# Kernel tuning notes

Hardware: AMD Instinct MI355X
Metric: run time of the kernel (lower is better)

The kernel has to match this reference:

```python
import jax, jax.numpy as jnp
import numpy as np

# static config (matches init_kwargs)
NH, NKV, E, K = 16, 4, 8, 2
CAP_FACTOR = 1.25
LN_EPS = 1e-5


def _layer_norm(x, w, b):
    mu = jnp.mean(x, axis=-1, keepdims=True)
    var = jnp.mean(jnp.square(x - mu), axis=-1, keepdims=True)
    return (x - mu) * jax.lax.rsqrt(var + LN_EPS) * w + b


def setup_inputs() -> dict:
    key = jax.random.key(0)
    ks = jax.random.split(key, 6)
    S, B, H, F = 2048, 1, 1024, 2048
    HD = H // NH
    qkv_out = NKV * ((NH // NKV) + 2) * HD  # 1536
    f32 = jnp.float32
    return {
        "hidden_states": jax.random.normal(ks[0], (S, B, H), f32),
        "ln1_weight": jnp.ones((H,), f32),
        "ln1_bias": jnp.zeros((H,), f32),
        "ln2_weight": jnp.ones((H,), f32),
        "ln2_bias": jnp.zeros((H,), f32),
        "qkv_weight": jax.random.normal(ks[1], (qkv_out, H), f32) * 0.02,
        "proj_weight": jax.random.normal(ks[2], (H, H), f32) * 0.02,
        "router_weight": jax.random.normal(ks[3], (H, E), f32) * 0.02,
        "moe_w1": jax.random.normal(ks[4], (E, H, F), f32) * 0.02,
        "moe_w2": jax.random.normal(ks[5], (F and E, F, H), f32)[:E] * 0.02 if False else jax.random.normal(ks[5], (E, F, H), f32) * 0.02,
    }


def reference(hidden_states, ln1_weight, ln1_bias, ln2_weight, ln2_bias,
              qkv_weight, proj_weight, router_weight, moe_w1, moe_w2):
    S, B, H = hidden_states.shape
    HD = H // NH
    q_per_kv = NH // NKV
    # ---- attention block (cp_size=1: all-to-alls are identity) ----
    ln1 = _layer_norm(hidden_states, ln1_weight, ln1_bias)
    qkv = jnp.einsum('sbh,oh->sbo', ln1, qkv_weight)
    qkv = qkv.reshape(S, B, NKV, (q_per_kv + 2) * HD)
    q = qkv[..., : q_per_kv * HD].reshape(S, B, NH, HD)
    k = qkv[..., q_per_kv * HD:(q_per_kv + 1) * HD]          # [S,B,NKV,HD]
    v = qkv[..., (q_per_kv + 1) * HD:]                        # [S,B,NKV,HD]
    qb = jnp.transpose(q, (1, 2, 0, 3)).reshape(B, NKV, q_per_kv, S, HD)
    kb = jnp.transpose(k, (1, 2, 0, 3))                       # [B,NKV,S,HD]
    vb = jnp.transpose(v, (1, 2, 0, 3))
    scale = 1.0 / np.sqrt(HD).astype(np.float32)
    scores = jnp.einsum('bgqsd,bgtd->bgqst', qb, kb) * scale  # [B,NKV,qpk,S,S]
    causal = jnp.tril(jnp.ones((S, S), bool))
    scores = jnp.where(causal, scores, jnp.finfo(scores.dtype).min)
    attn = jax.nn.softmax(scores, axis=-1)
    ao = jnp.einsum('bgqst,bgtd->bgqsd', attn, vb)
    ao = ao.reshape(B, NH, S, HD)
    ao = jnp.transpose(ao, (2, 0, 1, 3)).reshape(S, B, H)
    proj = jnp.einsum('sbh,oh->sbo', ao, proj_weight)
    h1 = hidden_states + proj
    # ---- MoE block (ep_size=1: uniform all-to-all is identity) ----
    ln2 = _layer_norm(h1, ln2_weight, ln2_bias)
    x = ln2.reshape(-1, H)                                    # [N,H]
    N = x.shape[0]
    logits = x @ router_weight                                # linear(x, router_weight.t())
    probs = jax.nn.softmax(logits, axis=-1)
    top_p, top_i = jax.lax.top_k(probs, K)
    top_p = top_p / jnp.sum(top_p, axis=-1, keepdims=True)
    exp_idx = top_i.reshape(-1)                               # [N*K]
    exp_p = top_p.reshape(-1)
    # stable sort by expert id, capacity-padded dispatch
    order = jnp.argsort(exp_idx, stable=True)
    sorted_exp = exp_idx[order]
    counts = jnp.bincount(exp_idx, length=E)
    offsets = jnp.concatenate([jnp.zeros((1,), counts.dtype), jnp.cumsum(counts)[:-1]])
    within = jnp.arange(N * K) - offsets[sorted_exp]
    cap = int(np.ceil(N * K / E * CAP_FACTOR))
    T = E * cap
    valid = within < cap
    dst = jnp.where(valid, sorted_exp * cap + within, T)      # T = out-of-bounds -> dropped
    padded_tokens = jnp.zeros((T, H), x.dtype).at[dst].set(x[order // K], mode='drop')
    padded_probs = jnp.zeros((T,), exp_p.dtype).at[dst].set(exp_p[order], mode='drop')
    padded_tid = jnp.zeros((T,), jnp.int32).at[dst].set((order // K).astype(jnp.int32), mode='drop')
    # grouped expert GEMMs: [E,cap,H] x [E,H,F] -> gelu -> [E,cap,H]
    xt = padded_tokens.reshape(E, cap, H)
    fc1 = jax.nn.gelu(jnp.einsum('ech,ehf->ecf', xt, moe_w1))
    fc2 = jnp.einsum('ecf,efh->ech', fc1, moe_w2).reshape(T, H)
    weighted = fc2 * padded_probs[:, None]                    # pad slots have prob 0
    moe_out = jnp.zeros((N, H), hidden_states.dtype).at[padded_tid].add(weighted)
    return h1 + moe_out.reshape(S, B, H)
```

## Files before the change

### kernel.cpp

```cpp
#include <hip/hip_runtime.h>
#include <hip/hip_bf16.h>
#include <stdint.h>

#define S_LEN 2048
#define HDIM  1024
#define NHEAD 16
#define NKVH  4
#define HEADD 64
#define QKV_O 1536
#define NEXP  8
#define TOPK  2
#define CAP   640
#define TCAP  (NEXP*CAP)
#define FDIM  2048
#define LOG2E 1.44269504088896f
#define NCHUNK 40
#define ATTN_BLOCKS (NCHUNK*NHEAD)
#define FUSED_TRANSP 3072

typedef __bf16 bf16x8 __attribute__((ext_vector_type(8)));
typedef float  f32x4  __attribute__((ext_vector_type(4)));
typedef unsigned int u32;
typedef u32 u32x4 __attribute__((ext_vector_type(4)));
typedef u32 u32x2 __attribute__((ext_vector_type(2)));
typedef unsigned short u16;
typedef u16 u16x8 __attribute__((ext_vector_type(8)));

__device__ __forceinline__ void gload16(const __bf16* g, __bf16* l) {
    __builtin_amdgcn_global_load_lds(
        (const __attribute__((address_space(1))) u32*)g,
        (__attribute__((address_space(3))) u32*)l, 16, 0, 0);
}

__device__ __constant__ const signed char c_strip[NCHUNK] =
    {0,1,2,3, 4,4, 5,5, 6,6, 7,7, 8,8,8, 9,9,9, 10,10,10, 11,11,11,
     12,12,12,12, 13,13,13,13, 14,14,14,14, 15,15,15,15};
__device__ __constant__ const signed char c_chunk[NCHUNK] =
    {0,0,0,0, 0,1, 0,1, 0,1, 0,1, 0,1,2, 0,1,2, 0,1,2, 0,1,2,
     0,1,2,3, 0,1,2,3, 0,1,2,3, 0,1,2,3};
__device__ __constant__ const signed char c_cbase[16] = {0,1,2,3,4,6,8,10,12,15,18,21,24,28,32,36};
__device__ __constant__ const signed char c_nch[16]   = {1,1,1,1,2,2,2,2,3,3,3,3,4,4,4,4};

__global__ __launch_bounds__(256)
void prep_kernel(const float* __restrict__ hidden, const float* __restrict__ ln1w,
                 const float* __restrict__ ln1bb, const float* __restrict__ qkvW,
                 const float* __restrict__ projW, __bf16* __restrict__ ln1o,
                 __bf16* __restrict__ projWb, __bf16* __restrict__ qkvWb) {
    const int b = blockIdx.x, tid = threadIdx.x;
    if (b < S_LEN) {
        __shared__ float red[256];
        const float* x = hidden + (size_t)b * HDIM;
        float xr[4];
        #pragma unroll
        for (int j = 0; j < 4; ++j) xr[j] = x[tid + 256*j];
        float s = xr[0] + xr[1] + xr[2] + xr[3];
        red[tid] = s; __syncthreads();
        for (int st = 128; st > 0; st >>= 1) { if (tid < st) red[tid] += red[tid+st]; __syncthreads(); }
        float mu = red[0] / HDIM; __syncthreads();
        float v = 0.f;
        #pragma unroll
        for (int j = 0; j < 4; ++j) { float d = xr[j]-mu; v += d*d; }
        red[tid] = v; __syncthreads();
        for (int st = 128; st > 0; st >>= 1) { if (tid < st) red[tid] += red[tid+st]; __syncthreads(); }
        float rstd = rsqrtf(red[0]/HDIM + 1e-5f);
        #pragma unroll
        for (int j = 0; j < 4; ++j) {
            int i = tid + 256*j;
            ln1o[(size_t)b*HDIM + i] = (__bf16)((xr[j]-mu)*rstd*ln1w[i] + ln1bb[i]);
        }
        return;
    }
    const float* src; __bf16* dst; int i;
    if (b < S_LEN + 768) { src = qkvW; dst = qkvWb; i = (b - S_LEN)*256 + tid; }
    else                 { src = projW; dst = projWb; i = (b - S_LEN - 768)*256 + tid; }
    const float4* s = (const float4*)src + (size_t)i*2;
    float4 a = s[0], b4 = s[1];
    __bf16 tmp[8] = {(__bf16)a.x,(__bf16)a.y,(__bf16)a.z,(__bf16)a.w,
                     (__bf16)b4.x,(__bf16)b4.y,(__bf16)b4.z,(__bf16)b4.w};
    *(u32x4*)(dst + (size_t)i*8) = *(u32x4*)tmp;
}

template<int EPI>
__global__ __launch_bounds__(256)
void gemm_bf16_kernel(const __bf16* __restrict__ A, const __bf16* __restrict__ Bt,
                      const float* __restrict__ R, void* __restrict__ Cout,
                      int N, int K, long sA, long sB, long sC) {
    __shared__ __bf16 As[128*64];
    __shared__ __bf16 Bs[128*64];
    const int e = blockIdx.z;
    A  += (size_t)e * sA;
    Bt += (size_t)e * sB;
    const int m0 = blockIdx.y*128, n0 = blockIdx.x*128;
    const int tid = threadIdx.x;
    const int lane = tid & 63, w = tid >> 6;
    const int lr = lane & 15, lg = lane >> 4;
    const int wr = w >> 1, wc = w & 1;
    const int srow8 = lane >> 3, sg = lane & 7;
    f32x4 acc[4][4] = {};
    for (int k0 = 0; k0 < K; k0 += 64) {
        __syncthreads();
        #pragma unroll
        for (int i = 0; i < 4; ++i) {
            int row = 32*w + 8*i + srow8;
            int src_g = sg ^ (row & 7);
            gload16(A  + (size_t)(m0+row)*K + k0 + src_g*8,
                    (__bf16*)((char*)As + (32*w + 8*i)*128));
            gload16(Bt + (size_t)(n0+row)*K + k0 + src_g*8,
                    (__bf16*)((char*)Bs + (32*w + 8*i)*128));
        }
        __syncthreads();
        #pragma unroll
        for (int ks = 0; ks < 2; ++ks) {
            bf16x8 af[4], bfr[4];
            #pragma unroll
            for (int mi = 0; mi < 4; ++mi) {
                int row = wr*64 + mi*16 + lr;
                af[mi] = *(const bf16x8*)((const char*)As + ((row*128 + (lg+4*ks)*16) ^ ((row&7)<<4)));
            }
            #pragma unroll
            for (int ni = 0; ni < 4; ++ni) {
                int row = wc*64 + ni*16 + lr;
                bfr[ni] = *(const bf16x8*)((const char*)Bs + ((row*128 + (lg+4*ks)*16) ^ ((row&7)<<4)));
            }
            #pragma unroll
            for (int mi = 0; mi < 4; ++mi)
                #pragma unroll
                for (int ni = 0; ni < 4; ++ni)
                    acc[mi][ni] = __builtin_amdgcn_mfma_f32_16x16x32_bf16(af[mi], bfr[ni], acc[mi][ni], 0,0,0);
        }
    }
    #pragma unroll
    for (int mi = 0; mi < 4; ++mi) {
        #pragma unroll
        for (int ni = 0; ni < 4; ++ni) {
            #pragma unroll
            for (int r = 0; r < 4; ++r) {
                int row = m0 + wr*64 + mi*16 + lg*4 + r;
                int col = n0 + wc*64 + ni*16 + lr;
                float v = acc[mi][ni][r];
                if (EPI == 1) v += R[(size_t)row*N + col];
                if (EPI == 2) {
                    float t = 0.7978845608028654f * (v + 0.044715f*v*v*v);
                    v = 0.5f * v * (1.f + tanhf(t));
                }
                if (EPI == 2 || EPI == 3)
                    ((__bf16*)Cout)[(size_t)e*sC + (size_t)row*N + col] = (__bf16)v;
                else
                    ((float*)Cout)[(size_t)e*sC + (size_t)row*N + col] = v;
            }
        }
    }
}

template<int EPI>
__global__ __launch_bounds__(256)
void gemm64_bf16_kernel(const __bf16* __restrict__ A, const __bf16* __restrict__ Bt,
                        const float* __restrict__ R, void* __restrict__ Cout,
                        int N, int K, long sA, long sB, long sC) {
    __shared__ __bf16 As[64*64];
    __shared__ __bf16 Bs[128*64];
    const int e = blockIdx.z;
    A  += (size_t)e * sA;
    Bt += (size_t)e * sB;
    const int m0 = blockIdx.y*64, n0 = blockIdx.x*128;
    const int tid = threadIdx.x;
    const int lane = tid & 63, w = tid >> 6;
    const int lr = lane & 15, lg = lane >> 4;
    const int srow8 = lane >> 3, sg = lane & 7;
    f32x4 acc[4][2] = {};
    for (int k0 = 0; k0 < K; k0 += 64) {
        __syncthreads();
        #pragma unroll
        for (int i = 0; i < 2; ++i) {
            int row = 16*w + 8*i + srow8;
            int src_g = sg ^ (row & 7);
            gload16(A + (size_t)(m0+row)*K + k0 + src_g*8,
                    (__bf16*)((char*)As + (16*w + 8*i)*128));
        }
        #pragma unroll
        for (int i = 0; i < 4; ++i) {
            int row = 32*w + 8*i + srow8;
            int src_g = sg ^ (row & 7);
            gload16(Bt + (size_t)(n0+row)*K + k0 + src_g*8,
                    (__bf16*)((char*)Bs + (32*w + 8*i)*128));
        }
        __syncthreads();
        #pragma unroll
        for (int ks = 0; ks < 2; ++ks) {
            bf16x8 af[4], bfr[2];
            #pragma unroll
            for (int mi = 0; mi < 4; ++mi) {
                int row = mi*16 + lr;
                af[mi] = *(const bf16x8*)((const char*)As + ((row*128 + (lg+4*ks)*16) ^ ((row&7)<<4)));
            }
            #pragma unroll
            for (int ni = 0; ni < 2; ++ni) {
                int row = w*32 + ni*16 + lr;
                bfr[ni] = *(const bf16x8*)((const char*)Bs + ((row*128 + (lg+4*ks)*16) ^ ((row&7)<<4)));
            }
            #pragma unroll
            for (int mi = 0; mi < 4; ++mi)
                #pragma unroll
                for (int ni = 0; ni < 2; ++ni)
                    acc[mi][ni] = __builtin_amdgcn_mfma_f32_16x16x32_bf16(af[mi], bfr[ni], acc[mi][ni], 0,0,0);
        }
    }
    #pragma unroll
    for (int mi = 0; mi < 4; ++mi) {
        #pragma unroll
        for (int ni = 0; ni < 2; ++ni) {
            #pragma unroll
            for (int r = 0; r < 4; ++r) {
                int row = m0 + mi*16 + lg*4 + r;
                int col = n0 + w*32 + ni*16 + lr;
                float v = acc[mi][ni][r];
                if (EPI == 1) v += R[(size_t)row*N + col];
                if (EPI == 2) {
                    float t = 0.7978845608028654f * (v + 0.044715f*v*v*v);
                    v = 0.5f * v * (1.f + tanhf(t));
                }
                if (EPI == 2 || EPI == 3)
                    ((__bf16*)Cout)[(size_t)e*sC + (size_t)row*N + col] = (__bf16)v;
                else
                    ((float*)Cout)[(size_t)e*sC + (size_t)row*N + col] = v;
            }
        }
    }
}

__global__ __launch_bounds__(256)
void proj_transp_kernel(const __bf16* __restrict__ A, const __bf16* __restrict__ Bt,
                        const float* __restrict__ R, float* __restrict__ Cout,
                        const float* __restrict__ w2, __bf16* __restrict__ w2t) {
    __shared__ __attribute__((aligned(16))) char smem[24576];
    const int bid = blockIdx.x, tid = threadIdx.x;
    if (bid >= 256) {
        float (*t)[65] = (float(*)[65])smem;
        const int tile = 6144 + (bid - 256);
        const int tt = tile - 4096;
        const int e = tt >> 9, rem = tt & 511;
        const int K = FDIM, N = HDIM;
        const int n0 = (rem & 15) * 64, k0 = (rem >> 4) * 64;
        const float* src = w2 + (size_t)e*K*N;
        __bf16* dst = w2t + (size_t)e*K*N;
        const int r = tid >> 4, c4 = (tid & 15) * 4;
        #pragma unroll
        for (int i = 0; i < 4; ++i) {
            float4 v = *(const float4*)(src + (size_t)(k0 + r + 16*i)*N + n0 + c4);
            t[r+16*i][c4+0] = v.x; t[r+16*i][c4+1] = v.y;
            t[r+16*i][c4+2] = v.z; t[r+16*i][c4+3] = v.w;
        }
        __syncthreads();
        const int rn = tid >> 3, kc = (tid & 7) * 8;
        #pragma unroll
        for (int i = 0; i < 2; ++i) {
            int n = rn + 32*i;
            __bf16 tmp[8];
            #pragma unroll
            for (int j = 0; j < 8; ++j) tmp[j] = (__bf16)t[kc+j][n];
            *(u32x4*)(dst + (size_t)(n0+n)*K + k0 + kc) = *(u32x4*)tmp;
        }
        return;
    }
    __bf16* As = (__bf16*)smem;
    __bf16* Bs = (__bf16*)(smem + 8192);
    const int N = HDIM, K = HDIM;
    const int m0 = (bid >> 3)*64, n0 = (bid & 7)*128;
    const int lane = tid & 63, w = tid >> 6;
    const int lr = lane & 15, lg = lane >> 4;
    const int srow8 = lane >> 3, sg = lane & 7;
    f32x4 acc[4][2] = {};
    for (int k0 = 0; k0 < K; k0 += 64) {
        __syncthreads();
        #pragma unroll
        for (int i = 0; i < 2; ++i) {
            int row = 16*w + 8*i + srow8;
            int src_g = sg ^ (row & 7);
            gload16(A + (size_t)(m0+row)*K + k0 + src_g*8,
                    (__bf16*)((char*)As + (16*w + 8*i)*128));
        }
        #pragma unroll
        for (int i = 0; i < 4; ++i) {
            int row = 32*w + 8*i + srow8;
            int src_g = sg ^ (row & 7);
            gload16(Bt + (size_t)(n0+row)*K + k0 + src_g*8,
                    (__bf16*)((char*)Bs + (32*w + 8*i)*128));
        }
        __syncthreads();
        #pragma unroll
        for (int ks = 0; ks < 2; ++ks) {
            bf16x8 af[4], bfr[2];
            #pragma unroll
            for (int mi = 0; mi < 4; ++mi) {
                int row = mi*16 + lr;
                af[mi] = *(const bf16x8*)((const char*)As + ((row*128 + (lg+4*ks)*16) ^ ((row&7)<<4)));
            }
            #pragma unroll
            for (int ni = 0; ni < 2; ++ni) {
                int row = w*32 + ni*16 + lr;
                bfr[ni] = *(const bf16x8*)((const char*)Bs + ((row*128 + (lg+4*ks)*16) ^ ((row&7)<<4)));
            }
            #pragma unroll
            for (int mi = 0; mi < 4; ++mi)
                #pragma unroll
                for (int ni = 0; ni < 2; ++ni)
                    acc[mi][ni] = __builtin_amdgcn_mfma_f32_16x16x32_bf16(af[mi], bfr[ni], acc[mi][ni], 0,0,0);
        }
    }
    #pragma unroll
    for (int mi = 0; mi < 4; ++mi) {
        #pragma unroll
        for (int ni = 0; ni < 2; ++ni) {
            #pragma unroll
            for (int r = 0; r < 4; ++r) {
                int row = m0 + mi*16 + lg*4 + r;
                int col = n0 + w*32 + ni*16 + lr;
                Cout[(size_t)row*N + col] = acc[mi][ni][r] + R[(size_t)row*N + col];
            }
        }
    }
}

__global__ __launch_bounds__(512)
void attn_transp_kernel(const __bf16* __restrict__ qkv, float* __restrict__ partO,
                        float* __restrict__ partML,
                        const float* __restrict__ w1, const float* __restrict__ w2,
                        __bf16* __restrict__ w1t, __bf16* __restrict__ w2t) {
    __shared__ __attribute__((aligned(16))) char smem[49152];
    const int bid = blockIdx.x;
    const bool is_attn = ((bid % 5) == 3) && (bid / 5 < ATTN_BLOCKS);

    if (!is_attn) {
        const int tb = bid - min(ATTN_BLOCKS, (bid + 2) / 5);
        const int half = threadIdx.x >> 8, t256 = threadIdx.x & 255;
        float (*t)[65] = (float(*)[65])(smem + half*16640);
        const int tile = tb*2 + half;
        const float* src; __bf16* dst; int K, N, n0, k0;
        if (tile < 4096) {
            int e = tile >> 9, rem = tile & 511;
            K = HDIM; N = FDIM; n0 = (rem & 31) * 64; k0 = (rem >> 5) * 64;
            src = w1 + (size_t)e*K*N; dst = w1t + (size_t)e*K*N;
        } else {
            int tt = tile - 4096; int e = tt >> 9, rem = tt & 511;
            K = FDIM; N = HDIM; n0 = (rem & 15) * 64; k0 = (rem >> 4) * 64;
            src = w2 + (size_t)e*K*N; dst = w2t + (size_t)e*K*N;
        }
        const int r = t256 >> 4, c4 = (t256 & 15) * 4;
        #pragma unroll
        for (int i = 0; i < 4; ++i) {
            float4 v = *(const float4*)(src + (size_t)(k0 + r + 16*i)*N + n0 + c4);
            t[r+16*i][c4+0] = v.x; t[r+16*i][c4+1] = v.y;
            t[r+16*i][c4+2] = v.z; t[r+16*i][c4+3] = v.w;
        }
        __syncthreads();
        const int rn = t256 >> 3, kc = (t256 & 7) * 8;
        #pragma unroll
        for (int i = 0; i < 2; ++i) {
            int n = rn + 32*i;
            __bf16 tmp[8];
            #pragma unroll
            for (int j = 0; j < 8; ++j) tmp[j] = (__bf16)t[kc+j][n];
            *(u32x4*)(dst + (size_t)(n0+n)*K + k0 + kc) = *(u32x4*)tmp;
        }
        return;
    }

    __bf16* Kls = (__bf16*)smem;
    __bf16* Vls = (__bf16*)(smem + 16384);
    const int a = bid / 5;
    const int cx = a % NCHUNK;
    const int h  = a / NCHUNK;
    const int hg = h >> 2, qi = h & 3;
    const int qb = c_strip[cx];
    const int t0 = 4 * c_chunk[cx];
    const int t1 = min(qb + 1, t0 + 4);
    const int q0 = qb * 128;
    const int tid  = threadIdx.x;
    const int w    = tid >> 6;
    const int lane = tid & 63;
    const int lr   = lane & 15;
    const int lg   = lane >> 4;

    const int krow = tid >> 2, kc = (tid & 3) * 2;
    const int va = tid & 63,  dg  = tid >> 6;
    u32x4 kreg[2]; u16x8 vreg[2];

    const __bf16* kbase = qkv + hg*384 + 256;
    const __bf16* vbase = qkv + hg*384 + 320;

#define ISSUE(T) do { \
        const __bf16* kp = kbase + (size_t)((T)*128 + krow)*QKV_O + kc*8; \
        kreg[0] = *(const u32x4*)(kp); \
        kreg[1] = *(const u32x4*)(kp + 8); \
        const __bf16* vp = vbase + (size_t)((T)*128 + 2*va)*QKV_O + dg*8; \
        vreg[0] = *(const u16x8*)(vp); \
        vreg[1] = *(const u16x8*)(vp + QKV_O); \
    } while(0)

#define COMMIT() do { \
        char* Kb = (char*)Kls; \
        *(u32x4*)(Kb + ((krow*128 + (kc+0)*16) ^ ((krow&7)<<4))) = kreg[0]; \
        *(u32x4*)(Kb + ((krow*128 + (kc+1)*16) ^ ((krow&7)<<4))) = kreg[1]; \
        char* Vb = (char*)Vls; \
        _Pragma("unroll") \
        for (int j = 0; j < 8; ++j) { \
            int d = dg*8 + j; \
            u32 u = ((u32)vreg[1][j] << 16) | vreg[0][j]; \
            *(u32*)(Vb + ((d*256 + va*4) ^ ((d&7)<<4))) = u; \
        } \
    } while(0)

    const int qrow = q0 + w*16 + lr;
    const __bf16* qp = qkv + (size_t)qrow*QKV_O + hg*384 + qi*64;
    bf16x8 qfrag[2];
    #pragma unroll
    for (int ks = 0; ks < 2; ++ks) {
        bf16x8 qr = *(const bf16x8*)(qp + ks*32 + lg*8);
        #pragma unroll
        for (int j = 0; j < 8; ++j) qfrag[ks][j] = (__bf16)((float)qr[j] * 0.125f);
    }
    bf16x8 ones;
    #pragma unroll
    for (int j = 0; j < 8; ++j) ones[j] = (__bf16)1.0f;

    f32x4 oacc[4] = {};
    f32x4 lcol = {};
    float mrow[4] = {-INFINITY,-INFINITY,-INFINITY,-INFINITY};

    ISSUE(t0);
    for (int t = t0; t < t1; ++t) {
        __syncthreads();
        COMMIT();
        if (t+1 < t1) ISSUE(t+1);
        __syncthreads();

        f32x4 sacc[8] = {};
        const char* Kb = (const char*)Kls;
        #pragma unroll
        for (int f = 0; f < 8; ++f) {
            int row = lr + 16*f;
            int swz = (row & 7) << 4;
            #pragma unroll
            for (int ks = 0; ks < 2; ++ks) {
                bf16x8 kf = *(const bf16x8*)(Kb + ((row*128 + (lg*8+32*ks)*2) ^ swz));
                sacc[f] = __builtin_amdgcn_mfma_f32_16x16x32_bf16(qfrag[ks], kf, sacc[f], 0,0,0);
            }
        }
        if (t == qb) {
            #pragma unroll
            for (int f = 0; f < 8; ++f)
                #pragma unroll
                for (int r = 0; r < 4; ++r)
                    if (lr + 16*f > 16*w + 4*lg + r) sacc[f][r] = -INFINITY;
        }
        float tm[4];
        #pragma unroll
        for (int r = 0; r < 4; ++r) {
            float a2 = fmaxf(fmaxf(sacc[0][r], sacc[1][r]), fmaxf(sacc[2][r], sacc[3][r]));
            float b2 = fmaxf(fmaxf(sacc[4][r], sacc[5][r]), fmaxf(sacc[6][r], sacc[7][r]));
            tm[r] = fmaxf(a2, b2);
        }
        #pragma unroll
        for (int msk = 1; msk < 16; msk <<= 1)
            #pragma unroll
            for (int r = 0; r < 4; ++r) tm[r] = fmaxf(tm[r], __shfl_xor(tm[r], msk, 64));
        float corr[4];
        #pragma unroll
        for (int r = 0; r < 4; ++r) {
            float mn = fmaxf(mrow[r], tm[r]);
            corr[r] = exp2f((mrow[r]-mn)*LOG2E);
            mrow[r] = mn;
        }
        #pragma unroll
        for (int f = 0; f < 8; ++f)
            #pragma unroll
            for (int r = 0; r < 4; ++r)
                sacc[f][r] = exp2f((sacc[f][r]-mrow[r])*LOG2E);
        #pragma unroll
        for (int ct = 0; ct < 4; ++ct)
            #pragma unroll
            for (int r = 0; r < 4; ++r) oacc[ct][r] *= corr[r];
        #pragma unroll
        for (int r = 0; r < 4; ++r) lcol[r] *= corr[r];

        char* Pw = smem + 32768 + w*2048;
        const char* Vb = (const char*)Vls;
        #pragma unroll
        for (int half = 0; half < 2; ++half) {
            #pragma unroll
            for (int f = 0; f < 4; ++f)
                #pragma unroll
                for (int r = 0; r < 4; ++r) {
                    int row = 4*lg + r, col = lr + 16*f;
                    *(__bf16*)(Pw + ((row*128 + col*2) ^ ((row&7)<<4))) = (__bf16)sacc[4*half+f][r];
                }
            bf16x8 pa[2];
            #pragma unroll
            for (int ks = 0; ks < 2; ++ks)
                pa[ks] = *(const bf16x8*)(Pw + ((lr*128 + (lg*8+32*ks)*2) ^ ((lr&7)<<4)));
            #pragma unroll
            for (int ks = 0; ks < 2; ++ks)
                lcol = __builtin_amdgcn_mfma_f32_16x16x32_bf16(pa[ks], ones, lcol, 0,0,0);
            #pragma unroll
            for (int ct = 0; ct < 4; ++ct) {
                int row = lr + 16*ct;
                int swz = (row & 7) << 4;
                #pragma unroll
                for (int ks = 0; ks < 2; ++ks) {
                    int gks = 2*half + ks;
                    bf16x8 vf = *(const bf16x8*)(Vb + ((row*256 + (lg*8+32*gks)*2) ^ swz));
                    oacc[ct] = __builtin_amdgcn_mfma_f32_16x16x32_bf16(pa[ks], vf, oacc[ct], 0,0,0);
                }
            }
        }
    }
    const int p = h*NCHUNK + cx;
    float* po = partO + (size_t)p * (128*64);
    #pragma unroll
    for (int ct = 0; ct < 4; ++ct)
        #pragma unroll
        for (int r = 0; r < 4; ++r)
            po[(16*w + 4*lg + r)*64 + 16*ct + lr] = oacc[ct][r];
    if (lr == 0) {
        float* pm = partML + (size_t)p * 256;
        #pragma unroll
        for (int r = 0; r < 4; ++r) {
            pm[(16*w + 4*lg + r)*2    ] = mrow[r];
            pm[(16*w + 4*lg + r)*2 + 1] = lcol[r];
        }
    }
#undef ISSUE
#undef COMMIT
}

__global__ __launch_bounds__(256)
void attn_combine_kernel(const float* __restrict__ partO, const float* __restrict__ partML,
                         __bf16* __restrict__ ao) {
    const int rb = blockIdx.x, h = blockIdx.y;
    const int row0 = rb*8;
    const int qb = row0 >> 7;
    const int nc = c_nch[qb], cb = c_cbase[qb];
    const int tid = threadIdx.x;
    const int rl = tid >> 5, d2 = (tid & 31) * 2;
    const int grow = row0 + rl;
    const int srow = grow & 127;
    const int pbase = h*NCHUNK + cb;
    float mv[4], lv[4];
    float M = -INFINITY;
    for (int c = 0; c < nc; ++c) {
        const float* pm = partML + (size_t)(pbase+c)*256 + srow*2;
        mv[c] = pm[0]; lv[c] = pm[1];
        M = fmaxf(M, mv[c]);
    }
    float L = 0.f, a0 = 0.f, a1 = 0.f;
    for (int c = 0; c < nc; ++c) {
        float wc = exp2f((mv[c]-M)*LOG2E);
        L += wc * lv[c];
        const float* po = partO + (size_t)(pbase+c)*(128*64) + srow*64 + d2;
        a0 += wc * po[0];
        a1 += wc * po[1];
    }
    float inv = 1.f / L;
    __bf16 o2[2] = {(__bf16)(a0*inv), (__bf16)(a1*inv)};
    *(u32*)(ao + (size_t)grow*HDIM + h*64 + d2) = *(u32*)o2;
}

__global__ __launch_bounds__(256)
void ln2_router_kernel(const float* __restrict__ h1, const float* __restrict__ w,
                       const float* __restrict__ b, const float* __restrict__ rw,
                       __bf16* __restrict__ x2b, int* __restrict__ expi,
                       float* __restrict__ expp) {
    const int t = blockIdx.x, tid = threadIdx.x;
    __shared__ float red[256];
    __shared__ float red8[256][8];
    const float* x = h1 + (size_t)t*HDIM;
    float xr[4];
    #pragma unroll
    for (int j = 0; j < 4; ++j) xr[j] = x[tid + 256*j];
    float s = xr[0] + xr[1] + xr[2] + xr[3];
    red[tid] = s; __syncthreads();
    for (int st = 128; st > 0; st >>= 1) { if (tid < st) red[tid] += red[tid+st]; __syncthreads(); }
    float mu = red[0] / HDIM; __syncthreads();
    float v = 0.f;
    #pragma unroll
    for (int j = 0; j < 4; ++j) { float d = xr[j]-mu; v += d*d; }
    red[tid] = v; __syncthreads();
    for (int st = 128; st > 0; st >>= 1) { if (tid < st) red[tid] += red[tid+st]; __syncthreads(); }
    float rstd = rsqrtf(red[0]/HDIM + 1e-5f);
    float part[8] = {};
    #pragma unroll
    for (int j = 0; j < 4; ++j) {
        int i = tid + 256*j;
        float o = (xr[j]-mu)*rstd*w[i] + b[i];
        x2b[(size_t)t*HDIM + i] = (__bf16)o;
        const float* wp = rw + (size_t)i*NEXP;
        #pragma unroll
        for (int e2 = 0; e2 < 8; ++e2) part[e2] += o * wp[e2];
    }
    #pragma unroll
    for (int e2 = 0; e2 < 8; ++e2) red8[tid][e2] = part[e2];
    __syncthreads();
    for (int st = 128; st > 0; st >>= 1) {
        if (tid < st)
            #pragma unroll
            for (int e2 = 0; e2 < 8; ++e2) red8[tid][e2] += red8[tid+st][e2];
        __syncthreads();
    }
    if (tid == 0) {
        float lg[8];
        #pragma unroll
        for (int e2 = 0; e2 < 8; ++e2) lg[e2] = red8[0][e2];
        int i0 = 0;
        for (int e2 = 1; e2 < 8; ++e2) if (lg[e2] > lg[i0]) i0 = e2;
        int i1 = -1;
        for (int e2 = 0; e2 < 8; ++e2) { if (e2 == i0) continue; if (i1 < 0 || lg[e2] > lg[i1]) i1 = e2; }
        float p1 = __expf(lg[i1] - lg[i0]);
        float inv = 1.f / (1.f + p1);
        expi[t*2]   = i0; expi[t*2+1] = i1;
        expp[t*2]   = inv; expp[t*2+1] = p1 * inv;
    }
}

__global__ __launch_bounds__(256)
void dst_fast_kernel(const int* __restrict__ expi, int* __restrict__ dst) {
    __shared__ int hist[256][9];
    const int tid = threadIdx.x;
    int ev[16];
    #pragma unroll
    for (int i = 0; i < 16; i += 4)
        *(int4*)(ev+i) = *(const int4*)(expi + tid*16 + i);
    int cnt[8] = {};
    #pragma unroll
    for (int i = 0; i < 16; ++i)
        #pragma unroll
        for (int e = 0; e < 8; ++e) cnt[e] += (ev[i] == e);
    #pragma unroll
    for (int e = 0; e < 8; ++e) hist[tid][e] = cnt[e];
    __syncthreads();
    const int w = tid >> 6, lane = tid & 63;
    #pragma unroll
    for (int rep = 0; rep < 2; ++rep) {
        int e = w + rep*4;
        int h0 = hist[4*lane+0][e], h1 = hist[4*lane+1][e],
            h2 = hist[4*lane+2][e], h3 = hist[4*lane+3][e];
        int s = h0+h1+h2+h3, inc = s;
        #pragma unroll
        for (int off = 1; off < 64; off <<= 1) {
            int v = __shfl_up(inc, off, 64);
            if (lane >= off) inc += v;
        }
        int excl = inc - s;
        hist[4*lane+0][e] = excl;
        hist[4*lane+1][e] = excl + h0;
        hist[4*lane+2][e] = excl + h0 + h1;
        hist[4*lane+3][e] = excl + h0 + h1 + h2;
    }
    __syncthreads();
    int run[8];
    #pragma unroll
    for (int e = 0; e < 8; ++e) run[e] = hist[tid][e];
    int out[16];
    #pragma unroll
    for (int i = 0; i < 16; ++i) {
        int e = ev[i], within = 0;
        #pragma unroll
        for (int e2 = 0; e2 < 8; ++e2)
            if (e == e2) { within = run[e2]; run[e2]++; }
        out[i] = (within < CAP) ? (e*CAP + within) : -1;
    }
    #pragma unroll
    for (int i = 0; i < 16; i += 4)
        *(int4*)(dst + tid*16 + i) = *(const int4*)(out+i);
}

__global__ void scatter_kernel(const __bf16* __restrict__ x2b, const int* __restrict__ dst,
                               __bf16* __restrict__ xt) {
    int s = blockIdx.x;
    int d = dst[s];
    if (d < 0) return;
    int t = s >> 1;
    int i = threadIdx.x;
    u32x2 v = *(const u32x2*)(x2b + (size_t)t*HDIM + i*4);
    *(u32x2*)(xt + (size_t)d*HDIM + i*4) = v;
}

__global__ void combine_kernel(const float* __restrict__ h1, const float* __restrict__ fc2,
                               const int* __restrict__ dst, const float* __restrict__ expp,
                               float* __restrict__ out) {
    int t = blockIdx.x;
    int d0 = dst[t*2], d1 = dst[t*2+1];
    float p0 = expp[t*2], p1 = expp[t*2+1];
    int i = threadIdx.x * 4;
    float4 v = *(const float4*)(h1 + (size_t)t*HDIM + i);
    if (d0 >= 0) {
        float4 f = *(const float4*)(fc2 + (size_t)d0*HDIM + i);
        v.x += p0*f.x; v.y += p0*f.y; v.z += p0*f.z; v.w += p0*f.w;
    }
    if (d1 >= 0) {
        float4 f = *(const float4*)(fc2 + (size_t)d1*HDIM + i);
        v.x += p1*f.x; v.y += p1*f.y; v.z += p1*f.z; v.w += p1*f.w;
    }
    *(float4*)(out + (size_t)t*HDIM + i) = v;
}

extern "C" void kernel_launch(void* const* d_in, const int* in_sizes, int n_in,
                              void* d_out, int out_size, void* d_ws, size_t ws_size,
                              hipStream_t stream) {
    const float* hidden = (const float*)d_in[0];
    const float* ln1w   = (const float*)d_in[1];
    const float* ln1b_  = (const float*)d_in[2];
    const float* ln2w   = (const float*)d_in[3];
    const float* ln2b_  = (const float*)d_in[4];
    const float* qkvW   = (const float*)d_in[5];
    const float* projW  = (const float*)d_in[6];
    const float* routW  = (const float*)d_in[7];
    const float* w1     = (const float*)d_in[8];
    const float* w2     = (const float*)d_in[9];
    float* out = (float*)d_out;

    char* base = (char*)d_ws;
    __bf16* w1t    = (__bf16*)(base);
    __bf16* w2t    = (__bf16*)(base + 33554432);
    __bf16* ln1b   = (__bf16*)(base);
    __bf16* qkvWb  = (__bf16*)(base + 4194304);
    char* B0 = base + 67108864;
    float*  h1   = (float*)(B0);
    __bf16* xtb  = (__bf16*)(B0 + 8388608);
    __bf16* fc1b = (__bf16*)(B0 + 18874368);
    float*  fc2  = (float*)(B0 + 39845888);
    __bf16* x2b    = (__bf16*)fc2;
    __bf16* qkvb   = (__bf16*)((char*)fc2 + 4194304);
    __bf16* aob    = (__bf16*)((char*)fc2 + 10485760);
    __bf16* projWb = (__bf16*)((char*)fc2 + 14680064);
    int*    expi = (int*)(B0 + 60817408);
    int*    dsts = (int*)(B0 + 60833792);
    float*  expp = (float*)(B0 + 60850176);
    float*  partML = (float*)xtb;
    float*  partO  = (float*)fc1b;

    prep_kernel<<<S_LEN + 768 + 512, 256, 0, stream>>>(
        hidden, ln1w, ln1b_, qkvW, projW, ln1b, projWb, qkvWb);
    gemm64_bf16_kernel<3><<<dim3(QKV_O/128, S_LEN/64, 1), 256, 0, stream>>>(
        ln1b, qkvWb, nullptr, qkvb, QKV_O, HDIM, 0, 0, 0);
    attn_transp_kernel<<<ATTN_BLOCKS + FUSED_TRANSP, 512, 0, stream>>>(
        qkvb, partO, partML, w1, w2, w1t, w2t);
    attn_combine_kernel<<<dim3(S_LEN/8, NHEAD), 256, 0, stream>>>(partO, partML, aob);
    proj_transp_kernel<<<256 + 2048, 256, 0, stream>>>(
        aob, projWb, hidden, h1, w2, w2t);
    ln2_router_kernel<<<S_LEN, 256, 0, stream>>>(h1, ln2w, ln2b_, routW, x2b, expi, expp);
    dst_fast_kernel<<<1, 256, 0, stream>>>(expi, dsts);
    scatter_kernel<<<S_LEN*TOPK, 256, 0, stream>>>(x2b, dsts, xtb);
    gemm_bf16_kernel<2><<<dim3(FDIM/128, CAP/128, NEXP), 256, 0, stream>>>(
        xtb, w1t, nullptr, fc1b, FDIM, HDIM,
        (long)CAP*HDIM, (long)FDIM*HDIM, (long)CAP*FDIM);
    gemm64_bf16_kernel<0><<<dim3(HDIM/128, CAP/64, NEXP), 256, 0, stream>>>(
        fc1b, w2t, nullptr, fc2, HDIM, FDIM,
        (long)CAP*FDIM, (long)FDIM*HDIM, (long)CAP*HDIM);
    combine_kernel<<<S_LEN, 256, 0, stream>>>(h1, fc2, dsts, expp, out);
}
```

Baseline: 222.0 us.

## Fuse QKV GEMM with weight transposes and store expert fc2 output as bf16

The standalone QKV GEMM is replaced by a combined kernel that interleaves its 384 GEMM tiles with 1024 w2 transpose tiles, so the weight conversion work is spread across three kernels (qkv, attention, proj) and overlaps with compute. The second expert GEMM now writes bf16 instead of fp32, and combine reads bf16, halving that intermediate's memory traffic. Workspace buffers are relaid out to fit the smaller fc2. The bf16 fc2 adds rounding error, and the transpose tile ranges must be partitioned exactly across the kernels.

Measured after the change: 221.4 us, median of 4. No clear change (-0.3%).

```diff
diff --git a/kernel.cpp b/kernel.cpp
--- a/kernel.cpp
+++ b/kernel.cpp
@@ -16,7 +16,7 @@
 #define LOG2E 1.44269504088896f
 #define NCHUNK 40
 #define ATTN_BLOCKS (NCHUNK*NHEAD)
-#define FUSED_TRANSP 3072
+#define ATTN_TRANSP 2560
 
 typedef __bf16 bf16x8 __attribute__((ext_vector_type(8)));
 typedef float  f32x4  __attribute__((ext_vector_type(4)));
@@ -40,6 +40,41 @@
      0,1,2,3, 0,1,2,3, 0,1,2,3, 0,1,2,3};
 __device__ __constant__ const signed char c_cbase[16] = {0,1,2,3,4,6,8,10,12,15,18,21,24,28,32,36};
 __device__ __constant__ const signed char c_nch[16]   = {1,1,1,1,2,2,2,2,3,3,3,3,4,4,4,4};
+
+__device__ __forceinline__ void transp_tile(const float* __restrict__ w1,
+                                            const float* __restrict__ w2,
+                                            __bf16* __restrict__ w1t,
+                                            __bf16* __restrict__ w2t,
+                                            int tile, int tid, char* smem) {
+    float (*t)[65] = (float(*)[65])smem;
+    const float* src; __bf16* dst; int K, N, n0, k0;
+    if (tile < 4096) {
+        int e = tile >> 9, rem = tile & 511;
+        K = HDIM; N = FDIM; n0 = (rem & 31) * 64; k0 = (rem >> 5) * 64;
+        src = w1 + (size_t)e*K*N; dst = w1t + (size_t)e*K*N;
+    } else {
+        int tt = tile - 4096; int e = tt >> 9, rem = tt & 511;
+        K = FDIM; N = HDIM; n0 = (rem & 15) * 64; k0 = (rem >> 4) * 64;
+        src = w2 + (size_t)e*K*N; dst = w2t + (size_t)e*K*N;
+    }
+    const int r = tid >> 4, c4 = (tid & 15) * 4;
+    #pragma unroll
+    for (int i = 0; i < 4; ++i) {
+        float4 v = *(const float4*)(src + (size_t)(k0 + r + 16*i)*N + n0 + c4);
+        t[r+16*i][c4+0] = v.x; t[r+16*i][c4+1] = v.y;
+        t[r+16*i][c4+2] = v.z; t[r+16*i][c4+3] = v.w;
+    }
+    __syncthreads();
+    const int rn = tid >> 3, kc = (tid & 7) * 8;
+    #pragma unroll
+    for (int i = 0; i < 2; ++i) {
+        int n = rn + 32*i;
+        __bf16 tmp[8];
+        #pragma unroll
+        for (int j = 0; j < 8; ++j) tmp[j] = (__bf16)t[kc+j][n];
+        *(u32x4*)(dst + (size_t)(n0+n)*K + k0 + kc) = *(u32x4*)tmp;
+    }
+}
 
 __global__ __launch_bounds__(256)
 void prep_kernel(const float* __restrict__ hidden, const float* __restrict__ ln1w,
@@ -229,37 +264,85 @@
 }
 
 __global__ __launch_bounds__(256)
+void qkv_transp_kernel(const __bf16* __restrict__ A, const __bf16* __restrict__ Bt,
+                       __bf16* __restrict__ Cout,
+                       const float* __restrict__ w1, const float* __restrict__ w2,
+                       __bf16* __restrict__ w1t, __bf16* __restrict__ w2t) {
+    __shared__ __attribute__((aligned(16))) char smem[24576];
+    const int bid = blockIdx.x, tid = threadIdx.x;
+    const bool is_gemm = ((bid % 3) == 1) && (bid / 3 < 384);
+    if (!is_gemm) {
+        const int tb = bid - min(384, (bid + 2) / 3);
+        transp_tile(w1, w2, w1t, w2t, 4096 + tb, tid, smem);
+        return;
+    }
+    __bf16* As = (__bf16*)smem;
+    __bf16* Bs = (__bf16*)(smem + 8192);
+    const int g = bid / 3;
+    const int N = QKV_O, K = HDIM;
+    const int m0 = (g / 12)*64, n0 = (g % 12)*128;
+    const int lane = tid & 63, w = tid >> 6;
+    const int lr = lane & 15, lg = lane >> 4;
+    const int srow8 = lane >> 3, sg = lane & 7;
+    f32x4 acc[4][2] = {};
+    for (int k0 = 0; k0 < K; k0 += 64) {
+        __syncthreads();
+        #pragma unroll
+        for (int i = 0; i < 2; ++i) {
+            int row = 16*w + 8*i + srow8;
+            int src_g = sg ^ (row & 7);
+            gload16(A + (size_t)(m0+row)*K + k0 + src_g*8,
+                    (__bf16*)((char*)As + (16*w + 8*i)*128));
+        }
+        #pragma unroll
+        for (int i = 0; i < 4; ++i) {
+            int row = 32*w + 8*i + srow8;
+            int src_g = sg ^ (row & 7);
+            gload16(Bt + (size_t)(n0+row)*K + k0 + src_g*8,
+                    (__bf16*)((char*)Bs + (32*w + 8*i)*128));
+        }
+        __syncthreads();
+        #pragma unroll
+        for (int ks = 0; ks < 2; ++ks) {
+            bf16x8 af[4], bfr[2];
+            #pragma unroll
+            for (int mi = 0; mi < 4; ++mi) {
+                int row = mi*16 + lr;
+                af[mi] = *(const bf16x8*)((const char*)As + ((row*128 + (lg+4*ks)*16) ^ ((row&7)<<4)));
+            }
+            #pragma unroll
+            for (int ni = 0; ni < 2; ++ni) {
+                int row = w*32 + ni*16 + lr;
+                bfr[ni] = *(const bf16x8*)((const char*)Bs + ((row*128 + (lg+4*ks)*16) ^ ((row&7)<<4)));
+            }
+            #pragma unroll
+            for (int mi = 0; mi < 4; ++mi)
+                #pragma unroll
+                for (int ni = 0; ni < 2; ++ni)
+                    acc[mi][ni] = __builtin_amdgcn_mfma_f32_16x16x32_bf16(af[mi], bfr[ni], acc[mi][ni], 0,0,0);
+        }
+    }
+    #pragma unroll
+    for (int mi = 0; mi < 4; ++mi)
+        #pragma unroll
+        for (int ni = 0; ni < 2; ++ni)
+            #pragma unroll
+            for (int r = 0; r < 4; ++r) {
+                int row = m0 + mi*16 + lg*4 + r;
+                int col = n0 + w*32 + ni*16 + lr;
+                Cout[(size_t)row*N + col] = (__bf16)acc[mi][ni][r];
+            }
+}
+
+__global__ __launch_bounds__(256)
 void proj_transp_kernel(const __bf16* __restrict__ A, const __bf16* __restrict__ Bt,
                         const float* __restrict__ R, float* __restrict__ Cout,
-                        const float* __restrict__ w2, __bf16* __restrict__ w2t) {
+                        const float* __restrict__ w1, const float* __restrict__ w2,
+                        __bf16* __restrict__ w1t, __bf16* __restrict__ w2t) {
     __shared__ __attribute__((aligned(16))) char smem[24576];
     const int bid = blockIdx.x, tid = threadIdx.x;
     if (bid >= 256) {
-        float (*t)[65] = (float(*)[65])smem;
-        const int tile = 6144 + (bid - 256);
-        const int tt = tile - 4096;
-        const int e = tt >> 9, rem = tt & 511;
-        const int K = FDIM, N = HDIM;
-        const int n0 = (rem & 15) * 64, k0 = (rem >> 4) * 64;
-        const float* src = w2 + (size_t)e*K*N;
-        __bf16* dst = w2t + (size_t)e*K*N;
-        const int r = tid >> 4, c4 = (tid & 15) * 4;
-        #pragma unroll
-        for (int i = 0; i < 4; ++i) {
-            float4 v = *(const float4*)(src + (size_t)(k0 + r + 16*i)*N + n0 + c4);
-            t[r+16*i][c4+0] = v.x; t[r+16*i][c4+1] = v.y;
-            t[r+16*i][c4+2] = v.z; t[r+16*i][c4+3] = v.w;
-        }
-        __syncthreads();
-        const int rn = tid >> 3, kc = (tid & 7) * 8;
-        #pragma unroll
-        for (int i = 0; i < 2; ++i) {
-            int n = rn + 32*i;
-            __bf16 tmp[8];
-            #pragma unroll
-            for (int j = 0; j < 8; ++j) tmp[j] = (__bf16)t[kc+j][n];
-            *(u32x4*)(dst + (size_t)(n0+n)*K + k0 + kc) = *(u32x4*)tmp;
-        }
+        transp_tile(w1, w2, w1t, w2t, 6144 + (bid - 256), tid, smem);
         return;
     }
     __bf16* As = (__bf16*)smem;
@@ -308,17 +391,15 @@
         }
     }
     #pragma unroll
-    for (int mi = 0; mi < 4; ++mi) {
-        #pragma unroll
-        for (int ni = 0; ni < 2; ++ni) {
+    for (int mi = 0; mi < 4; ++mi)
+        #pragma unroll
+        for (int ni = 0; ni < 2; ++ni)
             #pragma unroll
             for (int r = 0; r < 4; ++r) {
                 int row = m0 + mi*16 + lg*4 + r;
                 int col = n0 + w*32 + ni*16 + lr;
                 Cout[(size_t)row*N + col] = acc[mi][ni][r] + R[(size_t)row*N + col];
             }
-        }
-    }
 }
 
 __global__ __launch_bounds__(512)
@@ -333,35 +414,9 @@
     if (!is_attn) {
         const int tb = bid - min(ATTN_BLOCKS, (bid + 2) / 5);
         const int half = threadIdx.x >> 8, t256 = threadIdx.x & 255;
-        float (*t)[65] = (float(*)[65])(smem + half*16640);
-        const int tile = tb*2 + half;
-        const float* src; __bf16* dst; int K, N, n0, k0;
-        if (tile < 4096) {
-            int e = tile >> 9, rem = tile & 511;
-            K = HDIM; N = FDIM; n0 = (rem & 31) * 64; k0 = (rem >> 5) * 64;
-            src = w1 + (size_t)e*K*N; dst = w1t + (size_t)e*K*N;
-        } else {
-            int tt = tile - 4096; int e = tt >> 9, rem = tt & 511;
-            K = FDIM; N = HDIM; n0 = (rem & 15) * 64; k0 = (rem >> 4) * 64;
-            src = w2 + (size_t)e*K*N; dst = w2t + (size_t)e*K*N;
-        }
-        const int r = t256 >> 4, c4 = (t256 & 15) * 4;
-        #pragma unroll
-        for (int i = 0; i < 4; ++i) {
-            float4 v = *(const float4*)(src + (size_t)(k0 + r + 16*i)*N + n0 + c4);
-            t[r+16*i][c4+0] = v.x; t[r+16*i][c4+1] = v.y;
-            t[r+16*i][c4+2] = v.z; t[r+16*i][c4+3] = v.w;
-        }
-        __syncthreads();
-        const int rn = t256 >> 3, kc = (t256 & 7) * 8;
-        #pragma unroll
-        for (int i = 0; i < 2; ++i) {
-            int n = rn + 32*i;
-            __bf16 tmp[8];
-            #pragma unroll
-            for (int j = 0; j < 8; ++j) tmp[j] = (__bf16)t[kc+j][n];
-            *(u32x4*)(dst + (size_t)(n0+n)*K + k0 + kc) = *(u32x4*)tmp;
-        }
+        int tile0 = tb*2 + half;
+        int tile = (tile0 < 4096) ? tile0 : tile0 + 1024;
+        transp_tile(w1, w2, w1t, w2t, tile, t256, smem + half*16640);
         return;
     }
 
@@ -684,7 +739,7 @@
     *(u32x2*)(xt + (size_t)d*HDIM + i*4) = v;
 }
 
-__global__ void combine_kernel(const float* __restrict__ h1, const float* __restrict__ fc2,
+__global__ void combine_kernel(const float* __restrict__ h1, const __bf16* __restrict__ fc2b,
                                const int* __restrict__ dst, const float* __restrict__ expp,
                                float* __restrict__ out) {
     int t = blockIdx.x;
@@ -693,12 +748,16 @@
     int i = threadIdx.x * 4;
     float4 v = *(const float4*)(h1 + (size_t)t*HDIM + i);
     if (d0 >= 0) {
-        float4 f = *(const float4*)(fc2 + (size_t)d0*HDIM + i);
-        v.x += p0*f.x; v.y += p0*f.y; v.z += p0*f.z; v.w += p0*f.w;
+        u16x8 f; *(u32x2*)&f = *(const u32x2*)(fc2b + (size_t)d0*HDIM + i);
+        const __bf16* fb = (const __bf16*)&f;
+        v.x += p0*(float)fb[0]; v.y += p0*(float)fb[1];
+        v.z += p0*(float)fb[2]; v.w += p0*(float)fb[3];
     }
     if (d1 >= 0) {
-        float4 f = *(const float4*)(fc2 + (size_t)d1*HDIM + i);
-        v.x += p1*f.x; v.y += p1*f.y; v.z += p1*f.z; v.w += p1*f.w;
+        u16x8 f; *(u32x2*)&f = *(const u32x2*)(fc2b + (size_t)d1*HDIM + i);
+        const __bf16* fb = (const __bf16*)&f;
+        v.x += p1*(float)fb[0]; v.y += p1*(float)fb[1];
+        v.z += p1*(float)fb[2]; v.w += p1*(float)fb[3];
     }
     *(float4*)(out + (size_t)t*HDIM + i) = v;
 }
@@ -727,11 +786,11 @@
     float*  h1   = (float*)(B0);
     __bf16* xtb  = (__bf16*)(B0 + 8388608);
     __bf16* fc1b = (__bf16*)(B0 + 18874368);
-    float*  fc2  = (float*)(B0 + 39845888);
-    __bf16* x2b    = (__bf16*)fc2;
-    __bf16* qkvb   = (__bf16*)((char*)fc2 + 4194304);
-    __bf16* aob    = (__bf16*)((char*)fc2 + 10485760);
-    __bf16* projWb = (__bf16*)((char*)fc2 + 14680064);
+    __bf16* fc2b = (__bf16*)(B0 + 39845888);
+    __bf16* x2b    = (__bf16*)((char*)fc2b + 10485760);
+    __bf16* qkvb   = (__bf16*)((char*)fc2b + 14680064);
+    __bf16* aob    = (__bf16*)(B0 + 60817408 + 65536);
+    __bf16* projWb = (__bf16*)((char*)aob + 4194304);
     int*    expi = (int*)(B0 + 60817408);
     int*    dsts = (int*)(B0 + 60833792);
     float*  expp = (float*)(B0 + 60850176);
@@ -740,21 +799,21 @@
 
     prep_kernel<<<S_LEN + 768 + 512, 256, 0, stream>>>(
         hidden, ln1w, ln1b_, qkvW, projW, ln1b, projWb, qkvWb);
-    gemm64_bf16_kernel<3><<<dim3(QKV_O/128, S_LEN/64, 1), 256, 0, stream>>>(
-        ln1b, qkvWb, nullptr, qkvb, QKV_O, HDIM, 0, 0, 0);
-    attn_transp_kernel<<<ATTN_BLOCKS + FUSED_TRANSP, 512, 0, stream>>>(
+    qkv_transp_kernel<<<384 + 1024, 256, 0, stream>>>(
+        ln1b, qkvWb, qkvb, w1, w2, w1t, w2t);
+    attn_transp_kernel<<<ATTN_BLOCKS + ATTN_TRANSP, 512, 0, stream>>>(
         qkvb, partO, partML, w1, w2, w1t, w2t);
     attn_combine_kernel<<<dim3(S_LEN/8, NHEAD), 256, 0, stream>>>(partO, partML, aob);
     proj_transp_kernel<<<256 + 2048, 256, 0, stream>>>(
-        aob, projWb, hidden, h1, w2, w2t);
+        aob, projWb, hidden, h1, w1, w2, w1t, w2t);
     ln2_router_kernel<<<S_LEN, 256, 0, stream>>>(h1, ln2w, ln2b_, routW, x2b, expi, expp);
     dst_fast_kernel<<<1, 256, 0, stream>>>(expi, dsts);
     scatter_kernel<<<S_LEN*TOPK, 256, 0, stream>>>(x2b, dsts, xtb);
     gemm_bf16_kernel<2><<<dim3(FDIM/128, CAP/128, NEXP), 256, 0, stream>>>(
         xtb, w1t, nullptr, fc1b, FDIM, HDIM,
         (long)CAP*HDIM, (long)FDIM*HDIM, (long)CAP*FDIM);
-    gemm64_bf16_kernel<0><<<dim3(HDIM/128, CAP/64, NEXP), 256, 0, stream>>>(
-        fc1b, w2t, nullptr, fc2, HDIM, FDIM,
+    gemm64_bf16_kernel<3><<<dim3(HDIM/128, CAP/64, NEXP), 256, 0, stream>>>(
+        fc1b, w2t, nullptr, fc2b, HDIM, FDIM,
         (long)CAP*FDIM, (long)FDIM*HDIM, (long)CAP*HDIM);
-    combine_kernel<<<S_LEN, 256, 0, stream>>>(h1, fc2, dsts, expp, out);
-}
+    combine_kernel<<<S_LEN, 256, 0, stream>>>(h1, fc2b, dsts, expp, out);
+}
```
